# Optimization experiments

Measured on AMD Instinct MI355X. Metric: run time of the kernel, lower is better.

## Reference

```python
import jax, jax.numpy as jnp
import numpy as np
import math

F_DIM = 64
N_NODES = 2048
N_HEADS = 4
HEAD_DIM = F_DIM // N_HEADS
C_DIM = 8
FUSION_WEIGHT = 1e-05
LN_EPS = 1e-5
BATCH = 4


def setup_inputs() -> dict:
    key = jax.random.key(0)
    ks = jax.random.split(key, 16)

    def xavier(k, shape):
        fan_in, fan_out = shape[-2], shape[-1]
        lim = math.sqrt(6.0 / (fan_in + fan_out))
        return jax.random.uniform(k, shape, jnp.float32, -lim, lim)

    return {
        "features": jax.random.normal(ks[0], (BATCH, N_NODES, F_DIM), jnp.float32),
        "fixed_graph": jax.random.uniform(ks[1], (N_NODES, N_NODES), jnp.float32),
        "learned_graph": jax.random.uniform(ks[2], (BATCH, N_NODES, N_NODES), jnp.float32),
        # qkv_compress: Linear(F, 3C); qkv_expand: Linear(3C, 3F)
        "Wqc": xavier(ks[3], (F_DIM, 3 * C_DIM)),
        "bqc": jnp.zeros((3 * C_DIM,), jnp.float32),
        "Wqe": xavier(ks[4], (3 * C_DIM, 3 * F_DIM)),
        "bqe": jnp.zeros((3 * F_DIM,), jnp.float32),
        # output_compress: Linear(F, C); output_expand: Linear(C, F)
        "Woc": xavier(ks[5], (F_DIM, C_DIM)),
        "boc": jnp.zeros((C_DIM,), jnp.float32),
        "Woe": xavier(ks[6], (C_DIM, F_DIM)),
        "boe": jnp.zeros((F_DIM,), jnp.float32),
        # learned structure bias factors [H,N,C] @ [H,C,N]
        "bf1": xavier(ks[7], (N_HEADS, N_NODES, C_DIM)),
        "bf2": xavier(ks[8], (N_HEADS, C_DIM, N_NODES)),
        "graph_fusion": jnp.array([0.5], jnp.float32),
        "ln_g": jnp.ones((F_DIM,), jnp.float32),
        "ln_b": jnp.zeros((F_DIM,), jnp.float32),
    }


def _layernorm(x, g, b):
    mu = jnp.mean(x, axis=-1, keepdims=True)
    var = jnp.mean(jnp.square(x - mu), axis=-1, keepdims=True)
    return (x - mu) * jax.lax.rsqrt(var + LN_EPS) * g + b


def reference(features, fixed_graph, learned_graph, Wqc, bqc, Wqe, bqe,
              Woc, boc, Woe, boe, bf1, bf2, graph_fusion, ln_g, ln_b):
    B, N, F = features.shape
    H, hd = N_HEADS, HEAD_DIM
    residual = features

    # compressed QKV projection: [B,N,F] -> [B,N,3C] -> [B,N,3F]
    qkv = (features @ Wqc + bqc) @ Wqe + bqe
    q, k, v = jnp.split(qkv, 3, axis=-1)
    # [B,N,F] -> [B,H,N,hd]
    to_heads = lambda x: x.reshape(B, N, H, hd).transpose(0, 2, 1, 3)
    q, k, v = to_heads(q), to_heads(k), to_heads(v)

    # attention scores + learned low-rank structure bias [H,N,N]
    scores = jnp.einsum("bhnd,bhmd->bhnm", q, k) / math.sqrt(hd)
    scores = scores + jnp.einsum("hnc,hcm->hnm", bf1, bf2)

    # graph fusion: sigmoid-weighted blend of learned and fixed graphs
    fr = jax.nn.sigmoid(graph_fusion[0])
    combined = fr * learned_graph + (1.0 - fr) * fixed_graph[None, :, :]  # [B,N,N]
    scores = scores + combined[:, None, :, :]

    attn = jax.nn.softmax(scores, axis=-1)  # dropout is identity in eval mode
    context = jnp.einsum("bhnm,bhmd->bhnd", attn, v)
    context = context.transpose(0, 2, 1, 3).reshape(B, N, F)

    out = (context @ Woc + boc) @ Woe + boe
    out = _layernorm(out + residual, ln_g, ln_b)

    reg_loss = FUSION_WEIGHT * jnp.mean(jnp.abs(attn))
    return out, reg_loss
```

## Files before the change

### kernel.cpp

```cpp
#include <hip/hip_runtime.h>
#include <hip/hip_bf16.h>

#define BB 4
#define NN 2048
#define NH 4
#define HDD 16
#define FD 64
#define SPLIT 4
#define KPB (NN / SPLIT)
#define PADC 21
#define L2E 1.44269504088896f

typedef __attribute__((ext_vector_type(8))) short bf16x8;
typedef __attribute__((ext_vector_type(4))) float f32x4;

union BW { __hip_bfloat16 b; unsigned short u; };

static __device__ inline unsigned pk2(float a, float b) {
    BW x, y;
    x.b = __float2bfloat16(a);
    y.b = __float2bfloat16(b);
    return (unsigned)x.u | ((unsigned)y.u << 16);
}

static __device__ inline float wsum(float v) {
    v += __shfl_xor(v, 1);  v += __shfl_xor(v, 2);  v += __shfl_xor(v, 4);
    v += __shfl_xor(v, 8);  v += __shfl_xor(v, 16); v += __shfl_xor(v, 32);
    return v;
}

__global__ __launch_bounds__(64) void qkv_kernel(
    const float* __restrict__ feat,
    const float* __restrict__ Wqc, const float* __restrict__ bqc,
    const float* __restrict__ Wqe, const float* __restrict__ bqe,
    const float* __restrict__ bf1, const float* __restrict__ bf2,
    __hip_bfloat16* __restrict__ Qe, __hip_bfloat16* __restrict__ Ke,
    __hip_bfloat16* __restrict__ Vt)
{
    const int bn = blockIdx.x;
    const int b = bn >> 11, n = bn & (NN - 1);
    const int t = threadIdx.x;
    __shared__ float fv[FD];
    __shared__ float cc[24];

    fv[t] = feat[(size_t)bn * FD + t];
    __syncthreads();
    if (t < 24) {
        float a = bqc[t];
        #pragma unroll 8
        for (int d = 0; d < FD; ++d) a += fv[d] * Wqc[d * 24 + t];
        cc[t] = a;
    }
    __syncthreads();

    float v0 = bqe[t], v1 = bqe[t + 64], v2 = bqe[t + 128];
    #pragma unroll
    for (int j = 0; j < 24; ++j) {
        const float c = cc[j];
        v0 += c * Wqe[j * 192 + t];
        v1 += c * Wqe[j * 192 + 64 + t];
        v2 += c * Wqe[j * 192 + 128 + t];
    }
    const int h = t >> 4, hi = t & 15;
    const size_t rowQ = (((size_t)b * NH + h) * NN + n) * 32;
    Qe[rowQ + hi] = __float2bfloat16(v0 * (0.25f * L2E));
    Ke[rowQ + hi] = __float2bfloat16(v1);
    Vt[(((size_t)b * NH + h) * HDD + hi) * NN + n] = __float2bfloat16(v2);

    if (t < 32) {
        const int hh = t >> 3, c = t & 7;
        const size_t r = (((size_t)b * NH + hh) * NN + n) * 32;
        Qe[r + 16 + c] = __float2bfloat16(bf1[((size_t)hh * NN + n) * 8 + c] * L2E);
        Qe[r + 24 + c] = __float2bfloat16(0.f);
    } else {
        const int hh = (t - 32) >> 3, c = t & 7;
        const size_t r = (((size_t)b * NH + hh) * NN + n) * 32;
        Ke[r + 16 + c] = __float2bfloat16(bf2[((size_t)hh * 8 + c) * NN + n]);
        Ke[r + 24 + c] = __float2bfloat16(0.f);
    }
}

__global__ __launch_bounds__(256, 8) void attn_kernel(
    const float* __restrict__ fixedg, const float* __restrict__ learng,
    const float* __restrict__ gfus,
    const __hip_bfloat16* __restrict__ Qe, const __hip_bfloat16* __restrict__ Ke,
    const __hip_bfloat16* __restrict__ Vt,
    float* __restrict__ pacc, float* __restrict__ psum)
{
    __shared__ float ldsC[2][64 * PADC];
    __shared__ float ldsO[16][68];

    const int bid = blockIdx.x;
    const int split = bid & (SPLIT - 1);
    const int qt = (bid >> 2) & 127;
    const int b = bid >> 9;
    const int qb = qt << 4;
    const int kbase = split * KPB;
    const int t = threadIdx.x;
    const int hw = t >> 6;
    const int lane = t & 63;
    const int ql = lane & 15;
    const int g  = lane >> 4;

    const float sg = 1.f / (1.f + __expf(-gfus[0]));
    const float fre = sg * L2E, ofre = (1.f - sg) * L2E;

    const size_t bhN = ((size_t)b * NH + hw) * NN;
    const bf16x8 qf = *(const bf16x8*)(Qe + (bhN + qb + ql) * 32 + g * 8);
    const __hip_bfloat16* kptr = Ke + bhN * 32;
    const __hip_bfloat16* vbase = Vt + (((size_t)b * NH + hw) * HDD + ql) * NN;
    const int krow = 8 * (ql >> 2) + (ql & 3);

    const float* lbase = learng + ((size_t)b * NN + qb) * NN;
    const float* fbase = fixedg + (size_t)qb * NN;

    float ssum = 0.f;
    f32x4 acc = {0.f, 0.f, 0.f, 0.f};

#define STAGE(bufi, kt_) { \
    const int col = kbase + (kt_) * 64 + lane; \
    for (int qq = hw; qq < 16; qq += 4) \
        ldsC[bufi][lane * PADC + qq] = fre * lbase[(size_t)qq * NN + col] \
                                     + ofre * fbase[(size_t)qq * NN + col]; \
    }

    STAGE(0, 0);
    __syncthreads();

    for (int kt = 0; kt < KPB / 64; ++kt) {
        if (kt < KPB / 64 - 1) STAGE((kt & 1) ^ 1, kt + 1);
        const int buf = kt & 1;
        #pragma unroll
        for (int hf = 0; hf < 2; ++hf) {
            const int kb = kbase + kt * 64 + hf * 32;
            const bf16x8 k0 = *(const bf16x8*)(kptr + (size_t)(kb + krow) * 32 + g * 8);
            const bf16x8 k1 = *(const bf16x8*)(kptr + (size_t)(kb + 4 + krow) * 32 + g * 8);
            const f32x4 z = {0.f, 0.f, 0.f, 0.f};
            f32x4 c0 = __builtin_amdgcn_mfma_f32_16x16x32_bf16(k0, qf, z, 0, 0, 0);
            f32x4 c1 = __builtin_amdgcn_mfma_f32_16x16x32_bf16(k1, qf, z, 0, 0, 0);
            const int lk = hf * 32 + 8 * g;
            #pragma unroll
            for (int j = 0; j < 4; ++j) {
                c0[j] = __builtin_amdgcn_exp2f(c0[j] + ldsC[buf][(lk + j) * PADC + ql]);
                c1[j] = __builtin_amdgcn_exp2f(c1[j] + ldsC[buf][(lk + 4 + j) * PADC + ql]);
                ssum += c0[j] + c1[j];
            }
            union { unsigned u[4]; bf16x8 v; } pf;
            pf.u[0] = pk2(c0[0], c0[1]);
            pf.u[1] = pk2(c0[2], c0[3]);
            pf.u[2] = pk2(c1[0], c1[1]);
            pf.u[3] = pk2(c1[2], c1[3]);
            const bf16x8 vf = *(const bf16x8*)(vbase + kb + 8 * g);
            acc = __builtin_amdgcn_mfma_f32_16x16x32_bf16(vf, pf.v, acc, 0, 0, 0);
        }
        __syncthreads();
    }

    ssum += __shfl_xor(ssum, 16);
    ssum += __shfl_xor(ssum, 32);
    if (g == 0)
        psum[((size_t)(split * BB + b) * NH + hw) * NN + qb + ql] = ssum;

    #pragma unroll
    for (int j = 0; j < 4; ++j) ldsO[ql][hw * 16 + 4 * g + j] = acc[j];
    __syncthreads();
    for (int q2 = hw; q2 < 16; q2 += 4)
        pacc[((size_t)(split * BB + b) * NN + qb + q2) * FD + lane] = ldsO[q2][lane];
#undef STAGE
}

__global__ __launch_bounds__(256) void out_kernel(
    const float* __restrict__ pacc, const float* __restrict__ psum,
    const float* __restrict__ feat,
    const float* __restrict__ Woc, const float* __restrict__ boc,
    const float* __restrict__ Woe, const float* __restrict__ boe,
    const float* __restrict__ lng, const float* __restrict__ lnb,
    float* __restrict__ out)
{
    const int node = blockIdx.x * 4 + (threadIdx.x >> 6);
    const int d = threadIdx.x & 63;
    const int b = node >> 11, n = node & (NN - 1);
    const int h = d >> 4;
    float a = 0.f, sh = 0.f;
    #pragma unroll
    for (int sp = 0; sp < SPLIT; ++sp) {
        a  += pacc[((size_t)sp * BB * NN + node) * FD + d];
        sh += psum[((size_t)(sp * BB + b) * NH + h) * NN + n];
    }
    const float cv = a / sh;
    float c[8];
    #pragma unroll
    for (int j = 0; j < 8; ++j)
        c[j] = wsum(cv * Woc[d * 8 + j]) + boc[j];
    float o = boe[d];
    #pragma unroll
    for (int j = 0; j < 8; ++j) o += c[j] * Woe[j * 64 + d];
    o += feat[(size_t)node * FD + d];
    const float mu = wsum(o) * (1.f / 64.f);
    const float df = o - mu;
    const float va = wsum(df * df) * (1.f / 64.f);
    out[(size_t)node * FD + d] = df * rsqrtf(va + 1e-5f) * lng[d] + lnb[d];
    if (blockIdx.x == 0 && threadIdx.x == 0)
        out[(size_t)BB * NN * FD] = 4.8828125e-9f;
}

extern "C" void kernel_launch(void* const* d_in, const int* in_sizes, int n_in,
                              void* d_out, int out_size, void* d_ws, size_t ws_size,
                              hipStream_t stream) {
    const float* feat   = (const float*)d_in[0];
    const float* fixedg = (const float*)d_in[1];
    const float* learng = (const float*)d_in[2];
    const float* Wqc = (const float*)d_in[3];
    const float* bqc = (const float*)d_in[4];
    const float* Wqe = (const float*)d_in[5];
    const float* bqe = (const float*)d_in[6];
    const float* Woc = (const float*)d_in[7];
    const float* boc = (const float*)d_in[8];
    const float* Woe = (const float*)d_in[9];
    const float* boe = (const float*)d_in[10];
    const float* bf1 = (const float*)d_in[11];
    const float* bf2 = (const float*)d_in[12];
    const float* gfus = (const float*)d_in[13];
    const float* lng = (const float*)d_in[14];
    const float* lnb = (const float*)d_in[15];

    char* ws = (char*)d_ws;
    __hip_bfloat16* Qe = (__hip_bfloat16*)ws;
    __hip_bfloat16* Ke = Qe + (size_t)BB * NH * NN * 32;
    __hip_bfloat16* Vt = Ke + (size_t)BB * NH * NN * 32;
    float* pacc = (float*)(Vt + (size_t)BB * NH * HDD * NN);
    float* psum = pacc + (size_t)SPLIT * BB * NN * FD;
    float* out = (float*)d_out;

    hipLaunchKernelGGL(qkv_kernel, dim3(BB * NN), dim3(64), 0, stream,
                       feat, Wqc, bqc, Wqe, bqe, bf1, bf2, Qe, Ke, Vt);
    hipLaunchKernelGGL(attn_kernel, dim3(BB * (NN / 16) * SPLIT), dim3(256), 0, stream,
                       fixedg, learng, gfus, Qe, Ke, Vt, pacc, psum);
    hipLaunchKernelGGL(out_kernel, dim3(BB * NN / 4), dim3(256), 0, stream,
                       pacc, psum, feat, Woc, boc, Woe, boe, lng, lnb, out);
}
```

Before: 193.3 us.

## Load graph bias directly into registers, prefuse low-rank weights, batch per-node kernels

The attention kernel no longer stages the fused learned/fixed graph tile through double-buffered shared memory with block barriers. Each lane now reads its own row with vector loads straight from global memory and blends it in registers, and the launch-bounds occupancy hint drops from 8 to 6. A new small kernel multiplies the compress/expand weight pairs into single 64x192 and 64x64 matrices, so the QKV and output kernels each run one dense matvec, with 4 nodes per 256-thread block. The aim is to remove LDS traffic and barriers in the bandwidth-bound attention loop, at the cost of more scattered global access per lane and an extra launch.

```diff
diff --git a/kernel.cpp b/kernel.cpp
--- a/kernel.cpp
+++ b/kernel.cpp
@@ -8,7 +8,6 @@
 #define FD 64
 #define SPLIT 4
 #define KPB (NN / SPLIT)
-#define PADC 21
 #define L2E 1.44269504088896f
 
 typedef __attribute__((ext_vector_type(8))) short bf16x8;
@@ -29,65 +28,99 @@
     return v;
 }
 
-__global__ __launch_bounds__(64) void qkv_kernel(
-    const float* __restrict__ feat,
+__global__ __launch_bounds__(256) void fuse_kernel(
     const float* __restrict__ Wqc, const float* __restrict__ bqc,
     const float* __restrict__ Wqe, const float* __restrict__ bqe,
+    const float* __restrict__ Woc, const float* __restrict__ boc,
+    const float* __restrict__ Woe, const float* __restrict__ boe,
+    float* __restrict__ W1, float* __restrict__ b1,
+    float* __restrict__ W2, float* __restrict__ b2)
+{
+    const int t = threadIdx.x;
+    if (blockIdx.x == 0) {
+        for (int idx = t; idx < 64 * 192; idx += 256) {
+            const int r = idx / 192, c = idx - r * 192;
+            float a = 0.f;
+            #pragma unroll
+            for (int j = 0; j < 24; ++j) a += Wqc[r * 24 + j] * Wqe[j * 192 + c];
+            if (c < 64) a *= 0.25f * L2E;
+            W1[idx] = a;
+        }
+        if (t < 192) {
+            float a = bqe[t];
+            #pragma unroll
+            for (int j = 0; j < 24; ++j) a += bqc[j] * Wqe[j * 192 + t];
+            if (t < 64) a *= 0.25f * L2E;
+            b1[t] = a;
+        }
+    } else {
+        for (int idx = t; idx < 64 * 64; idx += 256) {
+            const int r = idx >> 6, c = idx & 63;
+            float a = 0.f;
+            #pragma unroll
+            for (int j = 0; j < 8; ++j) a += Woc[r * 8 + j] * Woe[j * 64 + c];
+            W2[idx] = a;
+        }
+        if (t < 64) {
+            float a = boe[t];
+            #pragma unroll
+            for (int j = 0; j < 8; ++j) a += boc[j] * Woe[j * 64 + t];
+            b2[t] = a;
+        }
+    }
+}
+
+__global__ __launch_bounds__(256) void qkv_kernel(
+    const float* __restrict__ feat,
+    const float* __restrict__ W1, const float* __restrict__ b1,
     const float* __restrict__ bf1, const float* __restrict__ bf2,
     __hip_bfloat16* __restrict__ Qe, __hip_bfloat16* __restrict__ Ke,
     __hip_bfloat16* __restrict__ Vt)
 {
-    const int bn = blockIdx.x;
+    __shared__ float fl[4][64];
+    const int t = threadIdx.x;
+    const int w = t >> 6, lane = t & 63;
+    const int bn = blockIdx.x * 4 + w;
     const int b = bn >> 11, n = bn & (NN - 1);
-    const int t = threadIdx.x;
-    __shared__ float fv[FD];
-    __shared__ float cc[24];
-
-    fv[t] = feat[(size_t)bn * FD + t];
+
+    fl[w][lane] = feat[(size_t)bn * FD + lane];
     __syncthreads();
-    if (t < 24) {
-        float a = bqc[t];
-        #pragma unroll 8
-        for (int d = 0; d < FD; ++d) a += fv[d] * Wqc[d * 24 + t];
-        cc[t] = a;
-    }
-    __syncthreads();
-
-    float v0 = bqe[t], v1 = bqe[t + 64], v2 = bqe[t + 128];
-    #pragma unroll
-    for (int j = 0; j < 24; ++j) {
-        const float c = cc[j];
-        v0 += c * Wqe[j * 192 + t];
-        v1 += c * Wqe[j * 192 + 64 + t];
-        v2 += c * Wqe[j * 192 + 128 + t];
-    }
-    const int h = t >> 4, hi = t & 15;
+
+    float v0 = b1[lane], v1 = b1[lane + 64], v2 = b1[lane + 128];
+    #pragma unroll 8
+    for (int d = 0; d < 64; ++d) {
+        const float f = fl[w][d];
+        v0 += f * W1[d * 192 + lane];
+        v1 += f * W1[d * 192 + 64 + lane];
+        v2 += f * W1[d * 192 + 128 + lane];
+    }
+
+    const int h = lane >> 4, hi = lane & 15;
     const size_t rowQ = (((size_t)b * NH + h) * NN + n) * 32;
-    Qe[rowQ + hi] = __float2bfloat16(v0 * (0.25f * L2E));
+    Qe[rowQ + hi] = __float2bfloat16(v0);
     Ke[rowQ + hi] = __float2bfloat16(v1);
     Vt[(((size_t)b * NH + h) * HDD + hi) * NN + n] = __float2bfloat16(v2);
 
-    if (t < 32) {
-        const int hh = t >> 3, c = t & 7;
+    if (lane < 32) {
+        const int hh = lane >> 3, c = lane & 7;
         const size_t r = (((size_t)b * NH + hh) * NN + n) * 32;
         Qe[r + 16 + c] = __float2bfloat16(bf1[((size_t)hh * NN + n) * 8 + c] * L2E);
         Qe[r + 24 + c] = __float2bfloat16(0.f);
     } else {
-        const int hh = (t - 32) >> 3, c = t & 7;
+        const int hh = (lane - 32) >> 3, c = lane & 7;
         const size_t r = (((size_t)b * NH + hh) * NN + n) * 32;
         Ke[r + 16 + c] = __float2bfloat16(bf2[((size_t)hh * 8 + c) * NN + n]);
         Ke[r + 24 + c] = __float2bfloat16(0.f);
     }
 }
 
-__global__ __launch_bounds__(256, 8) void attn_kernel(
+__global__ __launch_bounds__(256, 6) void attn_kernel(
     const float* __restrict__ fixedg, const float* __restrict__ learng,
     const float* __restrict__ gfus,
     const __hip_bfloat16* __restrict__ Qe, const __hip_bfloat16* __restrict__ Ke,
     const __hip_bfloat16* __restrict__ Vt,
     float* __restrict__ pacc, float* __restrict__ psum)
 {
-    __shared__ float ldsC[2][64 * PADC];
     __shared__ float ldsO[16][68];
 
     const int bid = blockIdx.x;
@@ -111,38 +144,31 @@
     const __hip_bfloat16* vbase = Vt + (((size_t)b * NH + hw) * HDD + ql) * NN;
     const int krow = 8 * (ql >> 2) + (ql & 3);
 
-    const float* lbase = learng + ((size_t)b * NN + qb) * NN;
-    const float* fbase = fixedg + (size_t)qb * NN;
+    const float* lrow = learng + ((size_t)b * NN + qb + ql) * NN + kbase;
+    const float* frow = fixedg + (size_t)(qb + ql) * NN + kbase;
 
     float ssum = 0.f;
     f32x4 acc = {0.f, 0.f, 0.f, 0.f};
 
-#define STAGE(bufi, kt_) { \
-    const int col = kbase + (kt_) * 64 + lane; \
-    for (int qq = hw; qq < 16; qq += 4) \
-        ldsC[bufi][lane * PADC + qq] = fre * lbase[(size_t)qq * NN + col] \
-                                     + ofre * fbase[(size_t)qq * NN + col]; \
-    }
-
-    STAGE(0, 0);
-    __syncthreads();
-
+    #pragma unroll 2
     for (int kt = 0; kt < KPB / 64; ++kt) {
-        if (kt < KPB / 64 - 1) STAGE((kt & 1) ^ 1, kt + 1);
-        const int buf = kt & 1;
         #pragma unroll
         for (int hf = 0; hf < 2; ++hf) {
+            const int co = kt * 64 + hf * 32 + 8 * g;
+            const f32x4 l0 = *(const f32x4*)(lrow + co);
+            const f32x4 l1 = *(const f32x4*)(lrow + co + 4);
+            const f32x4 f0 = *(const f32x4*)(frow + co);
+            const f32x4 f1 = *(const f32x4*)(frow + co + 4);
             const int kb = kbase + kt * 64 + hf * 32;
             const bf16x8 k0 = *(const bf16x8*)(kptr + (size_t)(kb + krow) * 32 + g * 8);
             const bf16x8 k1 = *(const bf16x8*)(kptr + (size_t)(kb + 4 + krow) * 32 + g * 8);
             const f32x4 z = {0.f, 0.f, 0.f, 0.f};
             f32x4 c0 = __builtin_amdgcn_mfma_f32_16x16x32_bf16(k0, qf, z, 0, 0, 0);
             f32x4 c1 = __builtin_amdgcn_mfma_f32_16x16x32_bf16(k1, qf, z, 0, 0, 0);
-            const int lk = hf * 32 + 8 * g;
             #pragma unroll
             for (int j = 0; j < 4; ++j) {
-                c0[j] = __builtin_amdgcn_exp2f(c0[j] + ldsC[buf][(lk + j) * PADC + ql]);
-                c1[j] = __builtin_amdgcn_exp2f(c1[j] + ldsC[buf][(lk + 4 + j) * PADC + ql]);
+                c0[j] = __builtin_amdgcn_exp2f(c0[j] + fre * l0[j] + ofre * f0[j]);
+                c1[j] = __builtin_amdgcn_exp2f(c1[j] + fre * l1[j] + ofre * f1[j]);
                 ssum += c0[j] + c1[j];
             }
             union { unsigned u[4]; bf16x8 v; } pf;
@@ -153,7 +179,6 @@
             const bf16x8 vf = *(const bf16x8*)(vbase + kb + 8 * g);
             acc = __builtin_amdgcn_mfma_f32_16x16x32_bf16(vf, pf.v, acc, 0, 0, 0);
         }
-        __syncthreads();
     }
 
     ssum += __shfl_xor(ssum, 16);
@@ -166,41 +191,41 @@
     __syncthreads();
     for (int q2 = hw; q2 < 16; q2 += 4)
         pacc[((size_t)(split * BB + b) * NN + qb + q2) * FD + lane] = ldsO[q2][lane];
-#undef STAGE
 }
 
 __global__ __launch_bounds__(256) void out_kernel(
     const float* __restrict__ pacc, const float* __restrict__ psum,
     const float* __restrict__ feat,
-    const float* __restrict__ Woc, const float* __restrict__ boc,
-    const float* __restrict__ Woe, const float* __restrict__ boe,
+    const float* __restrict__ W2, const float* __restrict__ b2,
     const float* __restrict__ lng, const float* __restrict__ lnb,
     float* __restrict__ out)
 {
-    const int node = blockIdx.x * 4 + (threadIdx.x >> 6);
-    const int d = threadIdx.x & 63;
+    __shared__ float cl[4][64];
+    const int t = threadIdx.x;
+    const int w = t >> 6, d = t & 63;
+    const int node = blockIdx.x * 4 + w;
     const int b = node >> 11, n = node & (NN - 1);
     const int h = d >> 4;
+
     float a = 0.f, sh = 0.f;
     #pragma unroll
     for (int sp = 0; sp < SPLIT; ++sp) {
         a  += pacc[((size_t)sp * BB * NN + node) * FD + d];
         sh += psum[((size_t)(sp * BB + b) * NH + h) * NN + n];
     }
-    const float cv = a / sh;
-    float c[8];
-    #pragma unroll
-    for (int j = 0; j < 8; ++j)
-        c[j] = wsum(cv * Woc[d * 8 + j]) + boc[j];
-    float o = boe[d];
-    #pragma unroll
-    for (int j = 0; j < 8; ++j) o += c[j] * Woe[j * 64 + d];
+    cl[w][d] = a / sh;
+    __syncthreads();
+
+    float o = b2[d];
+    #pragma unroll 8
+    for (int dd = 0; dd < 64; ++dd) o += cl[w][dd] * W2[dd * 64 + d];
     o += feat[(size_t)node * FD + d];
+
     const float mu = wsum(o) * (1.f / 64.f);
     const float df = o - mu;
     const float va = wsum(df * df) * (1.f / 64.f);
     out[(size_t)node * FD + d] = df * rsqrtf(va + 1e-5f) * lng[d] + lnb[d];
-    if (blockIdx.x == 0 && threadIdx.x == 0)
+    if (blockIdx.x == 0 && t == 0)
         out[(size_t)BB * NN * FD] = 4.8828125e-9f;
 }
 
@@ -230,12 +255,18 @@
     __hip_bfloat16* Vt = Ke + (size_t)BB * NH * NN * 32;
     float* pacc = (float*)(Vt + (size_t)BB * NH * HDD * NN);
     float* psum = pacc + (size_t)SPLIT * BB * NN * FD;
+    float* W1 = psum + (size_t)SPLIT * BB * NH * NN;
+    float* b1 = W1 + 64 * 192;
+    float* W2 = b1 + 192;
+    float* b2 = W2 + 64 * 64;
     float* out = (float*)d_out;
 
-    hipLaunchKernelGGL(qkv_kernel, dim3(BB * NN), dim3(64), 0, stream,
-                       feat, Wqc, bqc, Wqe, bqe, bf1, bf2, Qe, Ke, Vt);
+    hipLaunchKernelGGL(fuse_kernel, dim3(2), dim3(256), 0, stream,
+                       Wqc, bqc, Wqe, bqe, Woc, boc, Woe, boe, W1, b1, W2, b2);
+    hipLaunchKernelGGL(qkv_kernel, dim3(BB * NN / 4), dim3(256), 0, stream,
+                       feat, W1, b1, bf1, bf2, Qe, Ke, Vt);
     hipLaunchKernelGGL(attn_kernel, dim3(BB * (NN / 16) * SPLIT), dim3(256), 0, stream,
                        fixedg, learng, gfus, Qe, Ke, Vt, pacc, psum);
     hipLaunchKernelGGL(out_kernel, dim3(BB * NN / 4), dim3(256), 0, stream,
-                       pacc, psum, feat, Woc, boc, Woe, boe, lng, lnb, out);
-}
+                       pacc, psum, feat, W2, b2, lng, lnb, out);
+}
```

Measured after the change: 255.5 us. +32.1%, slower.
